# Kernel tuning notes

Measured on AMD Instinct MI355X. Metric: run time of the kernel, lower is better.

Reference implementation:

```python
import jax, jax.numpy as jnp
import numpy as np

EPS = 1e-15


def gmm_conv(x, edge_index, edge_attr, g, mu, sigma, root_w, bias):
    # PyG GMMConv (separate_gaussians=False, aggr='mean', root_weight=True)
    N = x.shape[0]
    K, D = mu.shape          # kernel_size, pseudo-coord dim
    M = bias.shape[0]        # out channels
    src, dst = edge_index[0], edge_index[1]
    xg = (x @ g).reshape(N, K, M)            # [N, K, M] transformed source feats
    x_j = xg[src]                            # [E, K, M] gather
    diff = edge_attr[:, None, :] - mu[None]  # [E, K, D]
    gauss = jnp.exp(jnp.sum(-0.5 * diff * diff / (EPS + sigma[None] ** 2), axis=-1))  # [E, K]
    msg = jnp.sum(x_j * gauss[:, :, None], axis=1)          # [E, M]
    agg = jax.ops.segment_sum(msg, dst, num_segments=N)     # scatter-sum
    cnt = jax.ops.segment_sum(jnp.ones((msg.shape[0], 1), msg.dtype), dst, num_segments=N)
    out = agg / jnp.maximum(cnt, 1.0)                        # scatter-mean (0 for isolated nodes)
    return out + x @ root_w + bias


def setup_inputs() -> dict:
    key = jax.random.key(0)
    ks = jax.random.split(key, 16)
    N, E, D, K = 100000, 1600000, 8, 1
    F_in, H, F_out = 32, 32, 32
    inp = {
        "edge_index": jax.random.randint(ks[0], (2, E), 0, N, dtype=jnp.int64)
        if jax.config.jax_enable_x64 else jax.random.randint(ks[0], (2, E), 0, N).astype(jnp.int32),
        "edge_weight": jax.random.normal(ks[1], (E, D), dtype=jnp.float32),
        "x": jax.random.normal(ks[2], (N, F_in), dtype=jnp.float32),
        # layer 1 params
        "g1": jax.random.normal(ks[3], (F_in, K * H), dtype=jnp.float32) * (1.0 / np.sqrt(F_in)),
        "mu1": jax.random.normal(ks[4], (K, D), dtype=jnp.float32),
        "sigma1": jnp.ones((K, D), dtype=jnp.float32),
        "root1": jax.random.normal(ks[5], (F_in, H), dtype=jnp.float32) * (1.0 / np.sqrt(F_in)),
        "b1": jnp.zeros((H,), dtype=jnp.float32),
        # layer 2 params
        "g2": jax.random.normal(ks[6], (H, K * F_out), dtype=jnp.float32) * (1.0 / np.sqrt(H)),
        "mu2": jax.random.normal(ks[7], (K, D), dtype=jnp.float32),
        "sigma2": jnp.ones((K, D), dtype=jnp.float32),
        "root2": jax.random.normal(ks[8], (H, F_out), dtype=jnp.float32) * (1.0 / np.sqrt(H)),
        "b2": jnp.zeros((F_out,), dtype=jnp.float32),
    }
    return inp


def reference(edge_index, edge_weight, x, g1, mu1, sigma1, root1, b1, g2, mu2, sigma2, root2, b2):
    h = gmm_conv(x, edge_index, edge_weight, g1, mu1, sigma1, root1, b1)
    out = gmm_conv(h, edge_index, edge_weight, g2, mu2, sigma2, root2, b2)
    return out
```

## Files before the change

kernel.cpp:

```cpp
#include <hip/hip_runtime.h>

#define F 32
#define D 8
#define BKN 512
#define BKSH 9
#define EPT 8
#define CAP 9216

typedef unsigned uv2 __attribute__((ext_vector_type(2)));
typedef float fv2 __attribute__((ext_vector_type(2)));
typedef float fv4 __attribute__((ext_vector_type(4)));

__device__ __forceinline__ unsigned f2bf(float f) {
    unsigned u = __float_as_uint(f);
    return (u + 0x7fffu + ((u >> 16) & 1u)) >> 16;
}
__device__ __forceinline__ float bf2f(unsigned b) {
    return __uint_as_float(b << 16);
}

__global__ void build_kernel(const int* __restrict__ ei, const float* __restrict__ ew,
                             const float* __restrict__ mu1, const float* __restrict__ sg1,
                             const float* __restrict__ mu2, const float* __restrict__ sg2,
                             int* __restrict__ bcur, uv2* __restrict__ bin, int NB, int E,
                             const float* __restrict__ x, const float* __restrict__ g1,
                             const float* __restrict__ root1, const float* __restrict__ b1,
                             unsigned short* __restrict__ xgh, float* __restrict__ xr,
                             int N, int binBlocks) {
    __shared__ int hist[512];
    __shared__ int cbase[512];
    __shared__ float gs[F * F];
    __shared__ float rs[F * F];
    int t = threadIdx.x;

    if ((int)blockIdx.x < binBlocks) {
        float m1v[D], i1[D], m2v[D], i2[D];
#pragma unroll
        for (int d = 0; d < D; ++d) {
            m1v[d] = mu1[d];
            i1[d] = -0.5f / (1e-15f + sg1[d] * sg1[d]);
            m2v[d] = mu2[d];
            i2[d] = -0.5f / (1e-15f + sg2[d] * sg2[d]);
        }
        if (t < NB) hist[t] = 0;
        __syncthreads();
        int e0 = blockIdx.x * (512 * EPT) + t;
        unsigned pks[EPT], gps[EPT];
        int bks[EPT];
#pragma unroll
        for (int k = 0; k < EPT; ++k) {
            int e = e0 + k * 512;
            bks[k] = -1;
            if (e < E) {
                int src = __builtin_nontemporal_load(&ei[e]);
                int dst = __builtin_nontemporal_load(&ei[E + e]);
                bks[k] = dst >> BKSH;
                pks[k] = (unsigned)src | ((unsigned)(dst & (BKN - 1)) << 20);
                const fv4* ew4 = (const fv4*)(ew + (size_t)e * D);
                fv4 w0 = __builtin_nontemporal_load(ew4);
                fv4 w1 = __builtin_nontemporal_load(ew4 + 1);
                float w[D] = {w0.x, w0.y, w0.z, w0.w, w1.x, w1.y, w1.z, w1.w};
                float s1 = 0.f, s2 = 0.f;
#pragma unroll
                for (int d = 0; d < D; ++d) {
                    float d1 = w[d] - m1v[d];
                    s1 += d1 * d1 * i1[d];
                    float d2 = w[d] - m2v[d];
                    s2 += d2 * d2 * i2[d];
                }
                gps[k] = f2bf(expf(s1)) | (f2bf(expf(s2)) << 16);
                atomicAdd(&hist[bks[k]], 1);
            }
        }
        __syncthreads();
        if (t < NB) {
            int c = hist[t];
            cbase[t] = t * CAP + (c ? atomicAdd(&bcur[t], c) : 0);
        }
        __syncthreads();
        if (t < NB) hist[t] = 0;
        __syncthreads();
#pragma unroll
        for (int k = 0; k < EPT; ++k) {
            if (bks[k] >= 0) {
                int pos = cbase[bks[k]] + atomicAdd(&hist[bks[k]], 1);
                if (pos < (bks[k] + 1) * CAP) {
                    uv2 p;
                    p.x = pks[k];
                    p.y = gps[k];
                    bin[pos] = p;
                }
            }
        }
    } else {
        for (int i = t; i < F * F; i += 512) {
            gs[i] = g1[i];
            rs[i] = root1[i];
        }
        __syncthreads();
        int m = t & 31;
        int node = (int)((((size_t)blockIdx.x - binBlocks) * 512 + t) >> 5);
        if (node >= N) return;
        float xv = x[(size_t)node * F + m];
        int base = t & 32;
        float accg = 0.f, accr = 0.f;
#pragma unroll
        for (int c = 0; c < F; ++c) {
            float xc = __shfl(xv, base + c, 64);
            accg += xc * gs[c * F + m];
            accr += xc * rs[c * F + m];
        }
        xgh[(size_t)node * F + m] = (unsigned short)f2bf(accg);
        xr[(size_t)node * F + m] = accr + b1[m];
    }
}

__global__ void csr_kernel(const uv2* __restrict__ bin, const int* __restrict__ bcur,
                           int2* __restrict__ off2, uv2* __restrict__ edata, int N) {
    int b = blockIdx.x;
    int ebase = b * CAP;
    int nE = min(bcur[b], CAP);
    __shared__ int cnt[BKN];
    __shared__ int cur[BKN];
    __shared__ int ps[BKN];
    int t = threadIdx.x;
    if (t < BKN) cnt[t] = 0;
    __syncthreads();
    for (int i = t; i < nE; i += 1024)
        atomicAdd(&cnt[(bin[ebase + i].x >> 20) & (BKN - 1)], 1);
    __syncthreads();
    int a = (t < BKN) ? cnt[t] : 0;
    if (t < BKN) ps[t] = a;
    __syncthreads();
    for (int d = 1; d < BKN; d <<= 1) {
        int u = (t < BKN && t >= d) ? ps[t - d] : 0;
        __syncthreads();
        if (t < BKN) ps[t] += u;
        __syncthreads();
    }
    if (t < BKN) {
        int excl = ps[t] - a;
        cur[t] = excl;
        int node = (b << BKSH) + t;
        if (node < N) {
            int2 o;
            o.x = ebase + excl;
            o.y = ebase + excl + a;
            off2[node] = o;
        }
    }
    __syncthreads();
    for (int i = t; i < nE; i += 1024) {
        uv2 p = bin[ebase + i];
        int dl = (p.x >> 20) & (BKN - 1);
        int pos = ebase + atomicAdd(&cur[dl], 1);
        uv2 q;
        q.x = p.x & 0xfffffu;
        q.y = p.y;
        edata[pos] = q;
    }
}

__global__ void agg1_fuse_kernel(const int2* __restrict__ off2,
                                 const uv2* __restrict__ edata,
                                 const unsigned* __restrict__ xg32,
                                 const fv2* __restrict__ xr2,
                                 const float* __restrict__ g2,
                                 const float* __restrict__ root2,
                                 const float* __restrict__ b2,
                                 unsigned* __restrict__ xg32_out,
                                 float2* __restrict__ xr2_out,
                                 int N) {
    __shared__ float gs[F * F];
    __shared__ float rs[F * F];
    for (int i = threadIdx.x; i < F * F; i += blockDim.x) {
        gs[i] = g2[i];
        rs[i] = root2[i];
    }
    __syncthreads();
    int t = threadIdx.x;
    int l = t & 15;
    int node = (int)((blockIdx.x * (size_t)blockDim.x + t) >> 4);
    if (node >= N) return;
    int base = t & 48;
    int2 so = off2[node];
    int s0 = so.x, s1 = so.y;
    int deg = s1 - s0;
    float a0 = 0.f, a1 = 0.f;
    for (int i = s0; i < s1; i += 16) {
        unsigned pk = 0;
        float gv = 0.f;
        if (i + l < s1) {
            uv2 ed = __builtin_nontemporal_load(&edata[i + l]);
            pk = ed.x;
            gv = bf2f(ed.y & 0xffffu);
        }
        unsigned xv[16];
        float gj[16];
#pragma unroll
        for (int j = 0; j < 16; ++j) {
            unsigned s = __shfl(pk, base + j, 64);
            gj[j] = __shfl(gv, base + j, 64);
            xv[j] = xg32[s * 16 + l];
        }
#pragma unroll
        for (int j = 0; j < 16; ++j) {
            a0 += bf2f(xv[j] & 0xffffu) * gj[j];
            a1 += __uint_as_float(xv[j] & 0xffff0000u) * gj[j];
        }
    }
    float inv = (deg > 0) ? 1.f / (float)deg : 0.f;
    fv2 r = __builtin_nontemporal_load(&xr2[(size_t)node * 16 + l]);
    float hx = a0 * inv + r.x;
    float hy = a1 * inv + r.y;
    float ag0 = 0.f, ag1 = 0.f, ar0 = 0.f, ar1 = 0.f;
#pragma unroll
    for (int c = 0; c < F; ++c) {
        float src = (c & 1) ? hy : hx;
        float hc = __shfl(src, base + (c >> 1), 64);
        ag0 += hc * gs[c * F + 2 * l];
        ag1 += hc * gs[c * F + 2 * l + 1];
        ar0 += hc * rs[c * F + 2 * l];
        ar1 += hc * rs[c * F + 2 * l + 1];
    }
    xg32_out[(size_t)node * 16 + l] = f2bf(ag0) | (f2bf(ag1) << 16);
    float2 xo;
    xo.x = ar0 + b2[2 * l];
    xo.y = ar1 + b2[2 * l + 1];
    xr2_out[(size_t)node * 16 + l] = xo;
}

__global__ void aggregate2_kernel(const int2* __restrict__ off2,
                                  const uv2* __restrict__ edata,
                                  const unsigned* __restrict__ xg32,
                                  const fv2* __restrict__ xr2,
                                  fv2* __restrict__ out2, int N) {
    int t = threadIdx.x;
    int l = t & 15;
    int node = (int)((blockIdx.x * (size_t)blockDim.x + t) >> 4);
    if (node >= N) return;
    int base = t & 48;
    int2 so = off2[node];
    int s0 = so.x, s1 = so.y;
    int deg = s1 - s0;
    float a0 = 0.f, a1 = 0.f;
    for (int i = s0; i < s1; i += 16) {
        unsigned pk = 0;
        float gv = 0.f;
        if (i + l < s1) {
            uv2 ed = __builtin_nontemporal_load(&edata[i + l]);
            pk = ed.x;
            gv = __uint_as_float(ed.y & 0xffff0000u);
        }
        unsigned xv[16];
        float gj[16];
#pragma unroll
        for (int j = 0; j < 16; ++j) {
            unsigned s = __shfl(pk, base + j, 64);
            gj[j] = __shfl(gv, base + j, 64);
            xv[j] = xg32[s * 16 + l];
        }
#pragma unroll
        for (int j = 0; j < 16; ++j) {
            a0 += bf2f(xv[j] & 0xffffu) * gj[j];
            a1 += __uint_as_float(xv[j] & 0xffff0000u) * gj[j];
        }
    }
    float inv = (deg > 0) ? 1.f / (float)deg : 0.f;
    fv2 r = __builtin_nontemporal_load(&xr2[(size_t)node * 16 + l]);
    fv2 o;
    o.x = a0 * inv + r.x;
    o.y = a1 * inv + r.y;
    __builtin_nontemporal_store(o, &out2[(size_t)node * 16 + l]);
}

extern "C" void kernel_launch(void* const* d_in, const int* in_sizes, int n_in,
                              void* d_out, int out_size, void* d_ws, size_t ws_size,
                              hipStream_t stream) {
    const int*   ei   = (const int*)d_in[0];
    const float* ew   = (const float*)d_in[1];
    const float* x    = (const float*)d_in[2];
    const float* g1   = (const float*)d_in[3];
    const float* mu1  = (const float*)d_in[4];
    const float* sg1  = (const float*)d_in[5];
    const float* r1   = (const float*)d_in[6];
    const float* b1   = (const float*)d_in[7];
    const float* g2   = (const float*)d_in[8];
    const float* mu2  = (const float*)d_in[9];
    const float* sg2  = (const float*)d_in[10];
    const float* r2   = (const float*)d_in[11];
    const float* b2   = (const float*)d_in[12];
    float* out = (float*)d_out;

    const int E = in_sizes[0] / 2;
    const int N = in_sizes[2] / F;
    const size_t NF = (size_t)N * F;
    const int NB = (N + BKN - 1) / BKN;

    uv2*            bin   = (uv2*)d_ws;
    uv2*            edata = bin + (size_t)NB * CAP;
    float*          xr1   = (float*)(edata + (size_t)NB * CAP);
    float*          xr2w  = xr1 + NF;
    unsigned short* xgh1  = (unsigned short*)(xr2w + NF);
    unsigned short* xgh2  = xgh1 + NF;
    int2*           off2  = (int2*)(xgh2 + NF);
    int*            bcur  = (int*)(off2 + N);

    const int BT = 256;
    const int blk_bin = (E + 512 * EPT - 1) / (512 * EPT);
    const int blk_tr  = (int)((NF + 511) / 512);
    const int blk_agg = (int)(((size_t)N * 16 + BT - 1) / BT);

    (void)hipMemsetAsync(bcur, 0, NB * sizeof(int), stream);

    build_kernel<<<blk_bin + blk_tr, 512, 0, stream>>>(
        ei, ew, mu1, sg1, mu2, sg2, bcur, bin, NB, E,
        x, g1, r1, b1, xgh1, xr1, N, blk_bin);

    csr_kernel<<<NB, 1024, 0, stream>>>(bin, bcur, off2, edata, N);

    agg1_fuse_kernel<<<blk_agg, BT, 0, stream>>>(off2, edata, (const unsigned*)xgh1,
                                                 (const fv2*)xr1, g2, r2, b2,
                                                 (unsigned*)xgh2, (float2*)xr2w, N);

    aggregate2_kernel<<<blk_agg, BT, 0, stream>>>(off2, edata, (const unsigned*)xgh2,
                                                  (const fv2*)xr2w, (fv2*)out, N);
}
```

Measured before the change: 233.7 us.

## Process two nodes per 16-lane group in aggregation kernels, halve bucket size

Each 16-lane group in both aggregation kernels now handles two destination nodes, interleaving their edge loops so more independent gathers are in flight per wave, and the fused transform reuses the shared-memory weight reads across both nodes. The binning bucket size drops from 512 to 256 nodes, with capacity halved to match, so the CSR build uses more, smaller buckets. The cost is more registers per thread, fewer waves launched, and wasted iterations when the two nodes' degrees differ. The first kernel also switches its edge loads from nontemporal to regular.

```diff
diff --git a/kernel.cpp b/kernel.cpp
--- a/kernel.cpp
+++ b/kernel.cpp
@@ -2,10 +2,10 @@
 
 #define F 32
 #define D 8
-#define BKN 512
-#define BKSH 9
+#define BKN 256
+#define BKSH 8
 #define EPT 8
-#define CAP 9216
+#define CAP 4608
 
 typedef unsigned uv2 __attribute__((ext_vector_type(2)));
 typedef float fv2 __attribute__((ext_vector_type(2)));
@@ -180,54 +180,101 @@
     __syncthreads();
     int t = threadIdx.x;
     int l = t & 15;
-    int node = (int)((blockIdx.x * (size_t)blockDim.x + t) >> 4);
-    if (node >= N) return;
+    int grp = (int)((blockIdx.x * (size_t)blockDim.x + t) >> 4);
+    int nA = 2 * grp, nB = 2 * grp + 1;
+    if (nA >= N) return;
+    bool hB = nB < N;
     int base = t & 48;
-    int2 so = off2[node];
-    int s0 = so.x, s1 = so.y;
-    int deg = s1 - s0;
-    float a0 = 0.f, a1 = 0.f;
-    for (int i = s0; i < s1; i += 16) {
-        unsigned pk = 0;
-        float gv = 0.f;
-        if (i + l < s1) {
-            uv2 ed = __builtin_nontemporal_load(&edata[i + l]);
-            pk = ed.x;
-            gv = bf2f(ed.y & 0xffffu);
-        }
-        unsigned xv[16];
-        float gj[16];
-#pragma unroll
-        for (int j = 0; j < 16; ++j) {
-            unsigned s = __shfl(pk, base + j, 64);
-            gj[j] = __shfl(gv, base + j, 64);
-            xv[j] = xg32[s * 16 + l];
-        }
-#pragma unroll
-        for (int j = 0; j < 16; ++j) {
-            a0 += bf2f(xv[j] & 0xffffu) * gj[j];
-            a1 += __uint_as_float(xv[j] & 0xffff0000u) * gj[j];
-        }
-    }
-    float inv = (deg > 0) ? 1.f / (float)deg : 0.f;
-    fv2 r = __builtin_nontemporal_load(&xr2[(size_t)node * 16 + l]);
-    float hx = a0 * inv + r.x;
-    float hy = a1 * inv + r.y;
-    float ag0 = 0.f, ag1 = 0.f, ar0 = 0.f, ar1 = 0.f;
+    int2 soA = off2[nA];
+    int2 soB = hB ? off2[nB] : soA;
+    if (!hB) { soB.y = soB.x; }
+    int sA0 = soA.x, sA1 = soA.y, sB0 = soB.x, sB1 = soB.y;
+    int degA = sA1 - sA0, degB = sB1 - sB0;
+    float a0A = 0.f, a1A = 0.f, a0B = 0.f, a1B = 0.f;
+    int iA = sA0, iB = sB0;
+    while (iA < sA1 || iB < sB1) {
+        unsigned pkA = 0, pkB = 0;
+        float gvA = 0.f, gvB = 0.f;
+        if (iA + l < sA1) {
+            uv2 ed = edata[iA + l];
+            pkA = ed.x;
+            gvA = bf2f(ed.y & 0xffffu);
+        }
+        if (iB + l < sB1) {
+            uv2 ed = edata[iB + l];
+            pkB = ed.x;
+            gvB = bf2f(ed.y & 0xffffu);
+        }
+        unsigned xvA[16], xvB[16];
+        float gjA[16], gjB[16];
+#pragma unroll
+        for (int j = 0; j < 16; ++j) {
+            unsigned s = __shfl(pkA, base + j, 64);
+            gjA[j] = __shfl(gvA, base + j, 64);
+            xvA[j] = xg32[s * 16 + l];
+        }
+#pragma unroll
+        for (int j = 0; j < 16; ++j) {
+            unsigned s = __shfl(pkB, base + j, 64);
+            gjB[j] = __shfl(gvB, base + j, 64);
+            xvB[j] = xg32[s * 16 + l];
+        }
+#pragma unroll
+        for (int j = 0; j < 16; ++j) {
+            a0A += bf2f(xvA[j] & 0xffffu) * gjA[j];
+            a1A += __uint_as_float(xvA[j] & 0xffff0000u) * gjA[j];
+        }
+#pragma unroll
+        for (int j = 0; j < 16; ++j) {
+            a0B += bf2f(xvB[j] & 0xffffu) * gjB[j];
+            a1B += __uint_as_float(xvB[j] & 0xffff0000u) * gjB[j];
+        }
+        iA += 16;
+        iB += 16;
+    }
+    float invA = (degA > 0) ? 1.f / (float)degA : 0.f;
+    float invB = (degB > 0) ? 1.f / (float)degB : 0.f;
+    fv2 rA = __builtin_nontemporal_load(&xr2[(size_t)nA * 16 + l]);
+    float hxA = a0A * invA + rA.x;
+    float hyA = a1A * invA + rA.y;
+    float hxB = 0.f, hyB = 0.f;
+    if (hB) {
+        fv2 rB = __builtin_nontemporal_load(&xr2[(size_t)nB * 16 + l]);
+        hxB = a0B * invB + rB.x;
+        hyB = a1B * invB + rB.y;
+    }
+    float ag0A = 0.f, ag1A = 0.f, ar0A = 0.f, ar1A = 0.f;
+    float ag0B = 0.f, ag1B = 0.f, ar0B = 0.f, ar1B = 0.f;
 #pragma unroll
     for (int c = 0; c < F; ++c) {
-        float src = (c & 1) ? hy : hx;
-        float hc = __shfl(src, base + (c >> 1), 64);
-        ag0 += hc * gs[c * F + 2 * l];
-        ag1 += hc * gs[c * F + 2 * l + 1];
-        ar0 += hc * rs[c * F + 2 * l];
-        ar1 += hc * rs[c * F + 2 * l + 1];
-    }
-    xg32_out[(size_t)node * 16 + l] = f2bf(ag0) | (f2bf(ag1) << 16);
-    float2 xo;
-    xo.x = ar0 + b2[2 * l];
-    xo.y = ar1 + b2[2 * l + 1];
-    xr2_out[(size_t)node * 16 + l] = xo;
+        float g0 = gs[c * F + 2 * l], g1v = gs[c * F + 2 * l + 1];
+        float r0 = rs[c * F + 2 * l], r1v = rs[c * F + 2 * l + 1];
+        float srcA = (c & 1) ? hyA : hxA;
+        float hcA = __shfl(srcA, base + (c >> 1), 64);
+        ag0A += hcA * g0;
+        ag1A += hcA * g1v;
+        ar0A += hcA * r0;
+        ar1A += hcA * r1v;
+        float srcB = (c & 1) ? hyB : hxB;
+        float hcB = __shfl(srcB, base + (c >> 1), 64);
+        ag0B += hcB * g0;
+        ag1B += hcB * g1v;
+        ar0B += hcB * r0;
+        ar1B += hcB * r1v;
+    }
+    float bx = b2[2 * l], by = b2[2 * l + 1];
+    xg32_out[(size_t)nA * 16 + l] = f2bf(ag0A) | (f2bf(ag1A) << 16);
+    float2 xoA;
+    xoA.x = ar0A + bx;
+    xoA.y = ar1A + by;
+    xr2_out[(size_t)nA * 16 + l] = xoA;
+    if (hB) {
+        xg32_out[(size_t)nB * 16 + l] = f2bf(ag0B) | (f2bf(ag1B) << 16);
+        float2 xoB;
+        xoB.x = ar0B + bx;
+        xoB.y = ar1B + by;
+        xr2_out[(size_t)nB * 16 + l] = xoB;
+    }
 }
 
 __global__ void aggregate2_kernel(const int2* __restrict__ off2,
@@ -237,41 +284,72 @@
                                   fv2* __restrict__ out2, int N) {
     int t = threadIdx.x;
     int l = t & 15;
-    int node = (int)((blockIdx.x * (size_t)blockDim.x + t) >> 4);
-    if (node >= N) return;
+    int grp = (int)((blockIdx.x * (size_t)blockDim.x + t) >> 4);
+    int nA = 2 * grp, nB = 2 * grp + 1;
+    if (nA >= N) return;
+    bool hB = nB < N;
     int base = t & 48;
-    int2 so = off2[node];
-    int s0 = so.x, s1 = so.y;
-    int deg = s1 - s0;
-    float a0 = 0.f, a1 = 0.f;
-    for (int i = s0; i < s1; i += 16) {
-        unsigned pk = 0;
-        float gv = 0.f;
-        if (i + l < s1) {
-            uv2 ed = __builtin_nontemporal_load(&edata[i + l]);
-            pk = ed.x;
-            gv = __uint_as_float(ed.y & 0xffff0000u);
-        }
-        unsigned xv[16];
-        float gj[16];
-#pragma unroll
-        for (int j = 0; j < 16; ++j) {
-            unsigned s = __shfl(pk, base + j, 64);
-            gj[j] = __shfl(gv, base + j, 64);
-            xv[j] = xg32[s * 16 + l];
-        }
-#pragma unroll
-        for (int j = 0; j < 16; ++j) {
-            a0 += bf2f(xv[j] & 0xffffu) * gj[j];
-            a1 += __uint_as_float(xv[j] & 0xffff0000u) * gj[j];
-        }
-    }
-    float inv = (deg > 0) ? 1.f / (float)deg : 0.f;
-    fv2 r = __builtin_nontemporal_load(&xr2[(size_t)node * 16 + l]);
-    fv2 o;
-    o.x = a0 * inv + r.x;
-    o.y = a1 * inv + r.y;
-    __builtin_nontemporal_store(o, &out2[(size_t)node * 16 + l]);
+    int2 soA = off2[nA];
+    int2 soB = hB ? off2[nB] : soA;
+    if (!hB) { soB.y = soB.x; }
+    int sA0 = soA.x, sA1 = soA.y, sB0 = soB.x, sB1 = soB.y;
+    int degA = sA1 - sA0, degB = sB1 - sB0;
+    float a0A = 0.f, a1A = 0.f, a0B = 0.f, a1B = 0.f;
+    int iA = sA0, iB = sB0;
+    while (iA < sA1 || iB < sB1) {
+        unsigned pkA = 0, pkB = 0;
+        float gvA = 0.f, gvB = 0.f;
+        if (iA + l < sA1) {
+            uv2 ed = __builtin_nontemporal_load(&edata[iA + l]);
+            pkA = ed.x;
+            gvA = __uint_as_float(ed.y & 0xffff0000u);
+        }
+        if (iB + l < sB1) {
+            uv2 ed = __builtin_nontemporal_load(&edata[iB + l]);
+            pkB = ed.x;
+            gvB = __uint_as_float(ed.y & 0xffff0000u);
+        }
+        unsigned xvA[16], xvB[16];
+        float gjA[16], gjB[16];
+#pragma unroll
+        for (int j = 0; j < 16; ++j) {
+            unsigned s = __shfl(pkA, base + j, 64);
+            gjA[j] = __shfl(gvA, base + j, 64);
+            xvA[j] = xg32[s * 16 + l];
+        }
+#pragma unroll
+        for (int j = 0; j < 16; ++j) {
+            unsigned s = __shfl(pkB, base + j, 64);
+            gjB[j] = __shfl(gvB, base + j, 64);
+            xvB[j] = xg32[s * 16 + l];
+        }
+#pragma unroll
+        for (int j = 0; j < 16; ++j) {
+            a0A += bf2f(xvA[j] & 0xffffu) * gjA[j];
+            a1A += __uint_as_float(xvA[j] & 0xffff0000u) * gjA[j];
+        }
+#pragma unroll
+        for (int j = 0; j < 16; ++j) {
+            a0B += bf2f(xvB[j] & 0xffffu) * gjB[j];
+            a1B += __uint_as_float(xvB[j] & 0xffff0000u) * gjB[j];
+        }
+        iA += 16;
+        iB += 16;
+    }
+    float invA = (degA > 0) ? 1.f / (float)degA : 0.f;
+    float invB = (degB > 0) ? 1.f / (float)degB : 0.f;
+    fv2 rA = __builtin_nontemporal_load(&xr2[(size_t)nA * 16 + l]);
+    fv2 oA;
+    oA.x = a0A * invA + rA.x;
+    oA.y = a1A * invA + rA.y;
+    __builtin_nontemporal_store(oA, &out2[(size_t)nA * 16 + l]);
+    if (hB) {
+        fv2 rB = __builtin_nontemporal_load(&xr2[(size_t)nB * 16 + l]);
+        fv2 oB;
+        oB.x = a0B * invB + rB.x;
+        oB.y = a1B * invB + rB.y;
+        __builtin_nontemporal_store(oB, &out2[(size_t)nB * 16 + l]);
+    }
 }
 
 extern "C" void kernel_launch(void* const* d_in, const int* in_sizes, int n_in,
@@ -309,7 +387,8 @@
     const int BT = 256;
     const int blk_bin = (E + 512 * EPT - 1) / (512 * EPT);
     const int blk_tr  = (int)((NF + 511) / 512);
-    const int blk_agg = (int)(((size_t)N * 16 + BT - 1) / BT);
+    const int nGrp    = (N + 1) / 2;
+    const int blk_agg = (int)(((size_t)nGrp * 16 + BT - 1) / BT);
 
     (void)hipMemsetAsync(bcur, 0, NB * sizeof(int), stream);
 
```

Result: slower. 312.0 us (+33.5%).

## Halve destination bucket size, use branchless edge loads and nontemporal stores

Applied to the files above, without the earlier changes.

Bucket width for the CSR build drops from 512 to 256 destination nodes, with the per-bucket capacity halved to match. This means more, smaller buckets handled by csr_kernel. The aggregation loops now load edge data unconditionally from a clamped index and mask the result, instead of branching around the load. The fused layer-1 kernel writes its outputs with nontemporal stores. Together these aim to cut divergence and cache pollution, at the cost of more blocks and a tighter overflow margin on the capacity.

```diff
diff --git a/kernel.cpp b/kernel.cpp
--- a/kernel.cpp
+++ b/kernel.cpp
@@ -2,10 +2,10 @@
 
 #define F 32
 #define D 8
-#define BKN 512
-#define BKSH 9
+#define BKN 256
+#define BKSH 8
 #define EPT 8
-#define CAP 9216
+#define CAP 4608
 
 typedef unsigned uv2 __attribute__((ext_vector_type(2)));
 typedef float fv2 __attribute__((ext_vector_type(2)));
@@ -169,7 +169,7 @@
                                  const float* __restrict__ root2,
                                  const float* __restrict__ b2,
                                  unsigned* __restrict__ xg32_out,
-                                 float2* __restrict__ xr2_out,
+                                 fv2* __restrict__ xr2_out,
                                  int N) {
     __shared__ float gs[F * F];
     __shared__ float rs[F * F];
@@ -188,13 +188,10 @@
     int deg = s1 - s0;
     float a0 = 0.f, a1 = 0.f;
     for (int i = s0; i < s1; i += 16) {
-        unsigned pk = 0;
-        float gv = 0.f;
-        if (i + l < s1) {
-            uv2 ed = __builtin_nontemporal_load(&edata[i + l]);
-            pk = ed.x;
-            gv = bf2f(ed.y & 0xffffu);
-        }
+        uv2 ed = __builtin_nontemporal_load(&edata[min(i + l, s1 - 1)]);
+        bool ok = (i + l < s1);
+        unsigned pk = ok ? ed.x : 0u;
+        float gv = ok ? bf2f(ed.y & 0xffffu) : 0.f;
         unsigned xv[16];
         float gj[16];
 #pragma unroll
@@ -223,11 +220,12 @@
         ar0 += hc * rs[c * F + 2 * l];
         ar1 += hc * rs[c * F + 2 * l + 1];
     }
-    xg32_out[(size_t)node * 16 + l] = f2bf(ag0) | (f2bf(ag1) << 16);
-    float2 xo;
+    unsigned og = f2bf(ag0) | (f2bf(ag1) << 16);
+    __builtin_nontemporal_store(og, &xg32_out[(size_t)node * 16 + l]);
+    fv2 xo;
     xo.x = ar0 + b2[2 * l];
     xo.y = ar1 + b2[2 * l + 1];
-    xr2_out[(size_t)node * 16 + l] = xo;
+    __builtin_nontemporal_store(xo, &xr2_out[(size_t)node * 16 + l]);
 }
 
 __global__ void aggregate2_kernel(const int2* __restrict__ off2,
@@ -245,13 +243,10 @@
     int deg = s1 - s0;
     float a0 = 0.f, a1 = 0.f;
     for (int i = s0; i < s1; i += 16) {
-        unsigned pk = 0;
-        float gv = 0.f;
-        if (i + l < s1) {
-            uv2 ed = __builtin_nontemporal_load(&edata[i + l]);
-            pk = ed.x;
-            gv = __uint_as_float(ed.y & 0xffff0000u);
-        }
+        uv2 ed = __builtin_nontemporal_load(&edata[min(i + l, s1 - 1)]);
+        bool ok = (i + l < s1);
+        unsigned pk = ok ? ed.x : 0u;
+        float gv = ok ? __uint_as_float(ed.y & 0xffff0000u) : 0.f;
         unsigned xv[16];
         float gj[16];
 #pragma unroll
@@ -321,7 +316,7 @@
 
     agg1_fuse_kernel<<<blk_agg, BT, 0, stream>>>(off2, edata, (const unsigned*)xgh1,
                                                  (const fv2*)xr1, g2, r2, b2,
-                                                 (unsigned*)xgh2, (float2*)xr2w, N);
+                                                 (unsigned*)xgh2, (fv2*)xr2w, N);
 
     aggregate2_kernel<<<blk_agg, BT, 0, stream>>>(off2, edata, (const unsigned*)xgh2,
                                                   (const fv2*)xr2w, (fv2*)out, N);
```

After: 239.6 us. 1.03x slower.
